# Optimization experiments

Measured on AMD Instinct MI355X. Metric: run time of the kernel, lower is better.

The kernel has to match this reference:

```python
import jax, jax.numpy as jnp
import numpy as np

N = 50000   # total nodes (50 graphs x 1000 nodes)
E = 500000  # total edges (avg degree 10)
G = 50      # number of graphs in the batch
IN = 128    # in_dim
H = 4       # attn_head
HID = [64, 128]  # graph_hiddens
SLOPE = 0.2      # negative_slope


def setup_inputs() -> dict:
    key = jax.random.key(0)
    ks = jax.random.split(key, 12)
    nodes_per_g = N // G
    edges_per_g = E // G
    # edges stay inside their own graph block (batched-graph structure)
    off = (jnp.arange(E) // edges_per_g) * nodes_per_g
    edge_src = (jax.random.randint(ks[0], (E,), 0, nodes_per_g) + off).astype(jnp.int32)
    edge_dst = (jax.random.randint(ks[1], (E,), 0, nodes_per_g) + off).astype(jnp.int32)
    node_graph = (jnp.arange(N) // nodes_per_g).astype(jnp.int32)

    def lin(k, i, o):
        return (jax.random.normal(k, (i, o), jnp.float32) / np.sqrt(i)).astype(jnp.float32)

    return dict(
        x=jax.random.normal(ks[2], (N, IN), jnp.float32),
        edge_src=edge_src, edge_dst=edge_dst, node_graph=node_graph,
        Wl1=lin(ks[3], IN, H * HID[0]), bl1=jnp.zeros((H * HID[0],), jnp.float32),
        Wr1=lin(ks[4], IN, H * HID[0]), br1=jnp.zeros((H * HID[0],), jnp.float32),
        attn1=jax.random.normal(ks[5], (H, HID[0]), jnp.float32) * 0.1,
        Wl2=lin(ks[6], HID[0], H * HID[1]), bl2=jnp.zeros((H * HID[1],), jnp.float32),
        Wr2=lin(ks[7], HID[0], H * HID[1]), br2=jnp.zeros((H * HID[1],), jnp.float32),
        attn2=jax.random.normal(ks[8], (H, HID[1]), jnp.float32) * 0.1,
        gate_w=lin(ks[9], HID[1], 1), gate_b=jnp.zeros((1,), jnp.float32),
    )


def _gat_layer(x, src, dst, Wl, bl, Wr, br, attn, n_heads, d_out):
    """DGL GATv2Conv (share_weights=False, no dropout) + maxpool over heads."""
    n = x.shape[0]
    fs = (x @ Wl + bl).reshape(n, n_heads, d_out)  # fc_src -> [N,H,D]
    fd = (x @ Wr + br).reshape(n, n_heads, d_out)  # fc_dst -> [N,H,D]
    # per-edge GATv2 logits: attn . leaky_relu(fs_u + fd_v)
    e = jax.nn.leaky_relu(fs[src] + fd[dst], SLOPE)      # [E,H,D]
    logits = jnp.einsum('ehd,hd->eh', e, attn)           # [E,H]
    # edge softmax over incoming edges of each destination node
    m = jax.ops.segment_max(logits, dst, num_segments=n)  # [N,H]
    a = jnp.exp(logits - m[dst])
    s = jax.ops.segment_sum(a, dst, num_segments=n)
    alpha = a / s[dst]                                   # [E,H]
    out = jax.ops.segment_sum(alpha[:, :, None] * fs[src], dst, num_segments=n)  # [N,H,D]
    # MaxPool1d(attn_head) over the head dimension -> [N,D]
    return out.max(axis=1)


def reference(x, edge_src, edge_dst, node_graph,
              Wl1, bl1, Wr1, br1, attn1,
              Wl2, bl2, Wr2, br2, attn2,
              gate_w, gate_b):
    h = _gat_layer(x, edge_src, edge_dst, Wl1, bl1, Wr1, br1, attn1, H, HID[0])
    h = _gat_layer(h, edge_src, edge_dst, Wl2, bl2, Wr2, br2, attn2, H, HID[1])
    # GlobalAttentionPooling: softmax(gate_nn(h)) per graph, weighted sum
    gate = (h @ gate_w + gate_b)[:, 0]                      # [N]
    gm = jax.ops.segment_max(gate, node_graph, num_segments=G)
    ga = jnp.exp(gate - gm[node_graph])
    gs = jax.ops.segment_sum(ga, node_graph, num_segments=G)
    alpha = (ga / gs[node_graph])[:, None]                  # [N,1]
    return jax.ops.segment_sum(alpha * h, node_graph, num_segments=G)  # [G, HID[1]]
```

## Files before the change

kernel.cpp:

```cpp
#include <hip/hip_runtime.h>
#include <hip/hip_bf16.h>


#define NN 50000
#define EE 500000
#define GG 50
#define NPG 1000
#define HH 4

typedef unsigned short ushort_t;
typedef unsigned int uint_t;
typedef __attribute__((ext_vector_type(8))) short bf16x8;
typedef __attribute__((ext_vector_type(4))) float f32x4;
typedef __attribute__((ext_vector_type(2))) float f32x2;

__device__ __forceinline__ ushort_t bf16r(float f) {
  __hip_bfloat16 h = __float2bfloat16(f);
  return *reinterpret_cast<ushort_t*>(&h);
}

__device__ __forceinline__ f32x2 up2v(uint_t u) {
  f32x2 r;
  r.x = __uint_as_float(u << 16);
  r.y = __uint_as_float(u & 0xffff0000u);
  return r;
}


__global__ void count_dst(const int* __restrict__ dst, int* __restrict__ counts) {
  int i = blockIdx.x * 256 + threadIdx.x;
  if (i < EE) atomicAdd(&counts[dst[i]], 1);
}

__global__ void scan_block(const int* __restrict__ in, int* __restrict__ out,
                           int* __restrict__ bsum, int n) {
  __shared__ int tmp[256];
  int t = threadIdx.x;
  int i = blockIdx.x * 256 + t;
  int v = (i < n) ? in[i] : 0;
  tmp[t] = v;
  __syncthreads();
  for (int off = 1; off < 256; off <<= 1) {
    int a = (t >= off) ? tmp[t - off] : 0;
    __syncthreads();
    tmp[t] += a;
    __syncthreads();
  }
  if (i < n) out[i] = tmp[t] - v;
  if (t == 255) bsum[blockIdx.x] = tmp[t];
}

__global__ void scan_bsum(int* __restrict__ bsum, int nb) {
  __shared__ int tmp[256];
  int t = threadIdx.x;
  int v = (t < nb) ? bsum[t] : 0;
  tmp[t] = v;
  __syncthreads();
  for (int off = 1; off < 256; off <<= 1) {
    int a = (t >= off) ? tmp[t - off] : 0;
    __syncthreads();
    tmp[t] += a;
    __syncthreads();
  }
  if (t < nb) bsum[t] = tmp[t] - v;
}

__global__ void scan_add(int* __restrict__ out, const int* __restrict__ bsum,
                         int* __restrict__ cursor, int n) {
  int i = blockIdx.x * 256 + threadIdx.x;
  if (i < n) {
    out[i] += bsum[blockIdx.x];
    cursor[i] = 0;
  }
}

__global__ void scatter_edges(const int* __restrict__ src, const int* __restrict__ dst,
                              const int* __restrict__ rowstart, int* __restrict__ cursor,
                              int* __restrict__ csr_src) {
  int i = blockIdx.x * 256 + threadIdx.x;
  if (i < EE) {
    int d = dst[i];
    int p = atomicAdd(&cursor[d], 1);
    csr_src[rowstart[d] + p] = src[i];
  }
}


__global__ void prep_w_all(const float* __restrict__ Wl1, const float* __restrict__ Wr1,
                           const float* __restrict__ Wl2, const float* __restrict__ Wr2,
                           ushort_t* __restrict__ BW1, ushort_t* __restrict__ BW2) {
  int i = blockIdx.x * 256 + threadIdx.x;
  if (i < 512 * 128) {
    int n = i >> 7, k = i & 127;
    const float* W = (n < 256) ? Wl1 : Wr1;
    BW1[i] = bf16r(W[(size_t)k * 256 + (n & 255)]);
  } else {
    int j = i - 512 * 128;
    int n = j >> 6, k = j & 63;
    const float* W = (n < 512) ? Wl2 : Wr2;
    BW2[j] = bf16r(W[(size_t)k * 512 + (n & 511)]);
  }
}


template<int KDIM, bool AF32>
__global__ __launch_bounds__(256)
void gemm_mfma(const float* __restrict__ Af, const ushort_t* __restrict__ Ab,
               const ushort_t* __restrict__ BW,
               const float* __restrict__ bl, const float* __restrict__ br, int nhalf,
               ushort_t* __restrict__ C, int nstride) {
  constexpr int RS = 72;
  __shared__ __align__(16) ushort_t As[128 * RS];
  __shared__ __align__(16) ushort_t Bs[128 * RS];
  const int t = threadIdx.x;
  const int m0 = blockIdx.x * 128, n0 = blockIdx.y * 128;
  const int lane = t & 63, wv = t >> 6;
  const int l16 = lane & 15, quad = lane >> 4;

  f32x4 acc[2][8];
#pragma unroll
  for (int b = 0; b < 2; ++b)
#pragma unroll
    for (int n = 0; n < 8; ++n) acc[b][n] = (f32x4){0.f, 0.f, 0.f, 0.f};

  for (int k0 = 0; k0 < KDIM; k0 += 64) {
    __syncthreads();
    if (AF32) {
      const int r = t >> 4, c4 = t & 15;
#pragma unroll
      for (int p = 0; p < 8; ++p) {
        int m = m0 + r + p * 16;
        int ms = (m < NN) ? m : NN - 1;
        float4 v = *(const float4*)(Af + (size_t)ms * KDIM + k0 + c4 * 4);
        uint2 pk;
        pk.x = (uint_t)bf16r(v.x) | ((uint_t)bf16r(v.y) << 16);
        pk.y = (uint_t)bf16r(v.z) | ((uint_t)bf16r(v.w) << 16);
        *(uint2*)(As + (r + p * 16) * RS + c4 * 4) = pk;
      }
    } else {
      const int r = t >> 3, seg = t & 7;
#pragma unroll
      for (int p = 0; p < 4; ++p) {
        int m = m0 + r + p * 32;
        int ms = (m < NN) ? m : NN - 1;
        *(uint4*)(As + (r + p * 32) * RS + seg * 8) =
            *(const uint4*)(Ab + (size_t)ms * KDIM + k0 + seg * 8);
      }
    }
    {
      const int r = t >> 3, seg = t & 7;
#pragma unroll
      for (int p = 0; p < 4; ++p) {
        *(uint4*)(Bs + (r + p * 32) * RS + seg * 8) =
            *(const uint4*)(BW + (size_t)(n0 + r + p * 32) * KDIM + k0 + seg * 8);
      }
    }
    __syncthreads();
#pragma unroll
    for (int kk = 0; kk < 2; ++kk) {
      bf16x8 a[2];
#pragma unroll
      for (int b = 0; b < 2; ++b)
        a[b] = *(const bf16x8*)(As + (wv * 32 + b * 16 + l16) * RS + kk * 32 + quad * 8);
#pragma unroll
      for (int n = 0; n < 8; ++n) {
        bf16x8 bb = *(const bf16x8*)(Bs + (n * 16 + l16) * RS + kk * 32 + quad * 8);
        acc[0][n] = __builtin_amdgcn_mfma_f32_16x16x32_bf16(a[0], bb, acc[0][n], 0, 0, 0);
        acc[1][n] = __builtin_amdgcn_mfma_f32_16x16x32_bf16(a[1], bb, acc[1][n], 0, 0, 0);
      }
    }
  }
  const float* bp = (n0 < nhalf) ? bl : br;
  const int nb = (n0 < nhalf) ? n0 : n0 - nhalf;
#pragma unroll
  for (int n = 0; n < 8; ++n) {
    const int col = n0 + n * 16 + l16;
    const float bv = bp[nb + n * 16 + l16];
#pragma unroll
    for (int b = 0; b < 2; ++b) {
      const int rowb = m0 + wv * 32 + b * 16 + quad * 4;
#pragma unroll
      for (int r = 0; r < 4; ++r) {
        if (rowb + r < NN)
          C[(size_t)(rowb + r) * nstride + col] = bf16r(acc[b][n][r] + bv);
      }
    }
  }
}


template<int N32> struct UV;
template<> struct UV<2> { typedef uint2 T; };
template<> struct UV<4> { typedef uint4 T; };

#define GAT_SLOTS ((NN / 4 + 7) / 8)
#define GAT_GRID  (GAT_SLOTS * 8)

template<int D, int STRIDE, bool OUTBF, bool GATE>
__global__ __launch_bounds__(256)
void gat_layer(const ushort_t* __restrict__ fsb, const ushort_t* __restrict__ fdb,
               const float* __restrict__ attn,
               const int* __restrict__ rowstart, const int* __restrict__ deg,
               const int* __restrict__ csr_src,
               float4* __restrict__ out4, ushort_t* __restrict__ outb,
               const float* __restrict__ gw, float* __restrict__ gate) {
  constexpr int DPL = D / 16;
  constexpr int NU  = DPL / 2;
  constexpr int NV4 = DPL / 4;
  constexpr int D4  = D / 4;
  typedef typename UV<NU>::T LT;

  const int b    = blockIdx.x;
  const int slot = (b & 7) * GAT_SLOTS + (b >> 3);
  if (slot >= NN / 4) return;
  const int lane = threadIdx.x & 63;
  const int wvid = threadIdx.x >> 6;
  const int v    = (slot << 2) + wvid;
  const int h    = lane >> 4;
  const int g16  = lane & 15;
  const int foff = h * D + g16 * DPL;

  f32x2 at2[NU], fd2[NU], gw2[NU];
  {
    const float* ap = attn + foff;
#pragma unroll
    for (int j = 0; j < NU; ++j) { at2[j].x = ap[2 * j]; at2[j].y = ap[2 * j + 1]; }
    LT raw = *reinterpret_cast<const LT*>(fdb + (size_t)v * STRIDE + foff);
    const uint_t* rw = reinterpret_cast<const uint_t*>(&raw);
#pragma unroll
    for (int j = 0; j < NU; ++j) fd2[j] = up2v(rw[j]);
    if constexpr (GATE) {
      const float* gp = gw + g16 * DPL;
#pragma unroll
      for (int j = 0; j < NU; ++j) { gw2[j].x = gp[2 * j]; gw2[j].y = gp[2 * j + 1]; }
    }
  }
  const int start = rowstart[v];
  const int n     = deg[v];
  const int* cp   = csr_src + start;

  float s = 0.f;
  f32x2 acc2[NU];
#pragma unroll
  for (int j = 0; j < NU; ++j) acc2[j] = (f32x2){0.f, 0.f};

  for (int e = 0; e < n; ++e) {
    const int u = cp[e];
    LT raw = *reinterpret_cast<const LT*>(fsb + (size_t)u * STRIDE + foff);
    const uint_t* rw = reinterpret_cast<const uint_t*>(&raw);
    f32x2 f0[NU];
#pragma unroll
    for (int j = 0; j < NU; ++j) f0[j] = up2v(rw[j]);
    f32x2 p2 = (f32x2){0.f, 0.f};
#pragma unroll
    for (int j = 0; j < NU; ++j) {
      f32x2 t = f0[j] + fd2[j];
      f32x2 l = __builtin_elementwise_max(t, t * 0.2f);
      p2 = __builtin_elementwise_fma(l, at2[j], p2);
    }
    float p = p2.x + p2.y;
    p += __shfl_xor(p, 1);
    p += __shfl_xor(p, 2);
    p += __shfl_xor(p, 4);
    p += __shfl_xor(p, 8);
    const float w = __expf(p);
    s += w;
    const f32x2 wv2 = {w, w};
#pragma unroll
    for (int j = 0; j < NU; ++j)
      acc2[j] = __builtin_elementwise_fma(wv2, f0[j], acc2[j]);
  }

  const float rs = (n > 0) ? (1.0f / s) : 0.f;
  float acc[DPL];
#pragma unroll
  for (int j = 0; j < NU; ++j) {
    acc[2 * j]     = acc2[j].x * rs;
    acc[2 * j + 1] = acc2[j].y * rs;
  }
#pragma unroll
  for (int i = 0; i < DPL; ++i) {
    acc[i] = fmaxf(acc[i], __shfl_xor(acc[i], 16));
    acc[i] = fmaxf(acc[i], __shfl_xor(acc[i], 32));
  }
  if constexpr (GATE) {
    f32x2 g2 = (f32x2){0.f, 0.f};
#pragma unroll
    for (int j = 0; j < NU; ++j) {
      f32x2 a2; a2.x = acc[2 * j]; a2.y = acc[2 * j + 1];
      g2 = __builtin_elementwise_fma(a2, gw2[j], g2);
    }
    float gp = g2.x + g2.y;
    gp += __shfl_xor(gp, 1);  gp += __shfl_xor(gp, 2);  gp += __shfl_xor(gp, 4);
    gp += __shfl_xor(gp, 8);  gp += __shfl_xor(gp, 16); gp += __shfl_xor(gp, 32);
    if (lane == 0) gate[v] = gp * 0.25f;
  }
  if (h == 0) {
    if constexpr (OUTBF) {
      ushort4 o;
      o.x = bf16r(acc[0]); o.y = bf16r(acc[1]); o.z = bf16r(acc[2]); o.w = bf16r(acc[3]);
      *reinterpret_cast<ushort4*>(outb + (size_t)v * D + g16 * 4) = o;
    } else {
#pragma unroll
      for (int i = 0; i < NV4; ++i)
        out4[(size_t)v * D4 + g16 * NV4 + i] =
            make_float4(acc[4 * i], acc[4 * i + 1], acc[4 * i + 2], acc[4 * i + 3]);
    }
  }
}


__global__ __launch_bounds__(256)
void pool_soft(const float* __restrict__ gate, float* __restrict__ alpha) {
  const int g = blockIdx.x, t = threadIdx.x;
  const int lane = t & 63, w = t >> 6;
  __shared__ float red[4];
  __shared__ float finm, fins;
  const float* gp = gate + g * NPG;

  float m = -__builtin_inff();
  for (int i = t; i < NPG; i += 256) m = fmaxf(m, gp[i]);
  m = fmaxf(m, __shfl_xor(m, 1));  m = fmaxf(m, __shfl_xor(m, 2));
  m = fmaxf(m, __shfl_xor(m, 4));  m = fmaxf(m, __shfl_xor(m, 8));
  m = fmaxf(m, __shfl_xor(m, 16)); m = fmaxf(m, __shfl_xor(m, 32));
  if (lane == 0) red[w] = m;
  __syncthreads();
  if (t == 0) finm = fmaxf(fmaxf(red[0], red[1]), fmaxf(red[2], red[3]));
  __syncthreads();
  const float gm = finm;

  float s = 0.f;
  for (int i = t; i < NPG; i += 256) s += __expf(gp[i] - gm);
  s += __shfl_xor(s, 1);  s += __shfl_xor(s, 2);  s += __shfl_xor(s, 4);
  s += __shfl_xor(s, 8);  s += __shfl_xor(s, 16); s += __shfl_xor(s, 32);
  if (lane == 0) red[w] = s;
  __syncthreads();
  if (t == 0) fins = 1.0f / (red[0] + red[1] + red[2] + red[3]);
  __syncthreads();
  const float inv = fins;

  for (int i = t; i < NPG; i += 256)
    alpha[g * NPG + i] = __expf(gp[i] - gm) * inv;
}

#define PCH 8
__global__ __launch_bounds__(128)
void pool_acc(const float* __restrict__ h2, const float* __restrict__ alpha,
              float* __restrict__ out) {
  const int g = blockIdx.x / PCH;
  const int c = blockIdx.x % PCH;
  const int d = threadIdx.x;
  const int n0 = g * NPG + c * (NPG / PCH);
  float acc = 0.f;
#pragma unroll 4
  for (int i = 0; i < NPG / PCH; ++i)
    acc = fmaf(alpha[n0 + i], h2[(size_t)(n0 + i) * 128 + d], acc);
  atomicAdd(&out[g * 128 + d], acc);
}


extern "C" void kernel_launch(void* const* d_in, const int* in_sizes, int n_in,
                              void* d_out, int out_size, void* d_ws, size_t ws_size,
                              hipStream_t stream) {
  const float* x        = (const float*)d_in[0];
  const int*   edge_src = (const int*)d_in[1];
  const int*   edge_dst = (const int*)d_in[2];
  const float* Wl1   = (const float*)d_in[4];
  const float* bl1   = (const float*)d_in[5];
  const float* Wr1   = (const float*)d_in[6];
  const float* br1   = (const float*)d_in[7];
  const float* attn1 = (const float*)d_in[8];
  const float* Wl2   = (const float*)d_in[9];
  const float* bl2   = (const float*)d_in[10];
  const float* Wr2   = (const float*)d_in[11];
  const float* br2   = (const float*)d_in[12];
  const float* attn2 = (const float*)d_in[13];
  const float* gate_w = (const float*)d_in[14];
  float* out = (float*)d_out;

  ushort_t* fsd1 = (ushort_t*)d_ws;
  ushort_t* fsd2 = fsd1;
  ushort_t* h1b  = fsd2 + (size_t)NN * 1024;
  float* h2      = (float*)(h1b + (size_t)NN * 64);
  float* gate    = h2 + (size_t)NN * 128;
  float* alpha   = gate + NN;
  ushort_t* BW1  = (ushort_t*)(alpha + NN);
  ushort_t* BW2  = BW1 + 512 * 128;
  int* counts   = (int*)(BW2 + 1024 * 64);
  int* rowstart = counts + NN;
  int* cursor   = rowstart + NN;
  int* csr_src  = cursor + NN;
  int* bsum     = csr_src + EE;

  hipMemsetAsync(counts, 0, NN * sizeof(int), stream);
  hipMemsetAsync(d_out, 0, (size_t)GG * 128 * sizeof(float), stream);

  const int nbN = (NN + 255) / 256;
  const int nbE = (EE + 255) / 256;
  const int MB  = (NN + 127) / 128;

  prep_w_all<<<(512 * 128 + 1024 * 64) / 256, 256, 0, stream>>>(
      Wl1, Wr1, Wl2, Wr2, BW1, BW2);

  count_dst<<<nbE, 256, 0, stream>>>(edge_dst, counts);
  scan_block<<<nbN, 256, 0, stream>>>(counts, rowstart, bsum, NN);
  scan_bsum<<<1, 256, 0, stream>>>(bsum, nbN);
  scan_add<<<nbN, 256, 0, stream>>>(rowstart, bsum, cursor, NN);
  scatter_edges<<<nbE, 256, 0, stream>>>(edge_src, edge_dst, rowstart, cursor, csr_src);

  gemm_mfma<128, true><<<dim3(MB, 4), 256, 0, stream>>>(
      x, nullptr, BW1, bl1, br1, 256, fsd1, 512);
  gat_layer<64, 512, true, false><<<GAT_GRID, 256, 0, stream>>>(
      fsd1, fsd1 + 256, attn1, rowstart, counts, csr_src,
      nullptr, h1b, nullptr, nullptr);
  gemm_mfma<64, false><<<dim3(MB, 8), 256, 0, stream>>>(
      nullptr, h1b, BW2, bl2, br2, 512, fsd2, 1024);
  gat_layer<128, 1024, false, true><<<GAT_GRID, 256, 0, stream>>>(
      fsd2, fsd2 + 512, attn2, rowstart, counts, csr_src,
      (float4*)h2, nullptr, gate_w, gate);

  pool_soft<<<GG, 256, 0, stream>>>(gate, alpha);
  pool_acc<<<GG * PCH, 128, 0, stream>>>(h2, alpha, out);
}
```

Before: 408.7 us.

## Fuse prep kernels and pooling kernels, prefetch neighbor rows in GAT loop

Merges the weight-conversion kernel into the degree-count kernel and merges the two pooling kernels into one 1024-thread kernel per graph. That kernel keeps alpha in shared memory and writes the output directly, so the alpha buffer, the output memset and the atomics are gone. The GAT edge loop now software-prefetches the next neighbor row and makes rowstart/deg wave-uniform with readfirstlane, and the gate weights are loaded late to reduce register pressure. The aim is fewer launches and better latency hiding. The cost is only 50 blocks for pooling and possibly more registers from the prefetch.

```diff
diff --git a/kernel.cpp b/kernel.cpp
--- a/kernel.cpp
+++ b/kernel.cpp
@@ -7,6 +7,8 @@
 #define GG 50
 #define NPG 1000
 #define HH 4
+#define NB_E ((EE + 255) / 256)
+#define NB_W 512
 
 typedef unsigned short ushort_t;
 typedef unsigned int uint_t;
@@ -27,10 +29,29 @@
 }
 
 
-__global__ void count_dst(const int* __restrict__ dst, int* __restrict__ counts) {
-  int i = blockIdx.x * 256 + threadIdx.x;
-  if (i < EE) atomicAdd(&counts[dst[i]], 1);
-}
+__global__ void prep_count(const int* __restrict__ dst, int* __restrict__ counts,
+                           const float* __restrict__ Wl1, const float* __restrict__ Wr1,
+                           const float* __restrict__ Wl2, const float* __restrict__ Wr2,
+                           ushort_t* __restrict__ BW1, ushort_t* __restrict__ BW2) {
+  const int b = blockIdx.x;
+  if (b < NB_E) {
+    int i = b * 256 + threadIdx.x;
+    if (i < EE) atomicAdd(&counts[dst[i]], 1);
+  } else {
+    int i = (b - NB_E) * 256 + threadIdx.x;
+    if (i < 512 * 128) {
+      int n = i >> 7, k = i & 127;
+      const float* W = (n < 256) ? Wl1 : Wr1;
+      BW1[i] = bf16r(W[(size_t)k * 256 + (n & 255)]);
+    } else {
+      int j = i - 512 * 128;
+      int n = j >> 6, k = j & 63;
+      const float* W = (n < 512) ? Wl2 : Wr2;
+      BW2[j] = bf16r(W[(size_t)k * 512 + (n & 511)]);
+    }
+  }
+}
+
 
 __global__ void scan_block(const int* __restrict__ in, int* __restrict__ out,
                            int* __restrict__ bsum, int n) {
@@ -82,23 +103,6 @@
     int d = dst[i];
     int p = atomicAdd(&cursor[d], 1);
     csr_src[rowstart[d] + p] = src[i];
-  }
-}
-
-
-__global__ void prep_w_all(const float* __restrict__ Wl1, const float* __restrict__ Wr1,
-                           const float* __restrict__ Wl2, const float* __restrict__ Wr2,
-                           ushort_t* __restrict__ BW1, ushort_t* __restrict__ BW2) {
-  int i = blockIdx.x * 256 + threadIdx.x;
-  if (i < 512 * 128) {
-    int n = i >> 7, k = i & 127;
-    const float* W = (n < 256) ? Wl1 : Wr1;
-    BW1[i] = bf16r(W[(size_t)k * 256 + (n & 255)]);
-  } else {
-    int j = i - 512 * 128;
-    int n = j >> 6, k = j & 63;
-    const float* W = (n < 512) ? Wl2 : Wr2;
-    BW2[j] = bf16r(W[(size_t)k * 512 + (n & 511)]);
   }
 }
 
@@ -220,7 +224,7 @@
   const int g16  = lane & 15;
   const int foff = h * D + g16 * DPL;
 
-  f32x2 at2[NU], fd2[NU], gw2[NU];
+  f32x2 at2[NU], fd2[NU];
   {
     const float* ap = attn + foff;
 #pragma unroll
@@ -229,14 +233,9 @@
     const uint_t* rw = reinterpret_cast<const uint_t*>(&raw);
 #pragma unroll
     for (int j = 0; j < NU; ++j) fd2[j] = up2v(rw[j]);
-    if constexpr (GATE) {
-      const float* gp = gw + g16 * DPL;
-#pragma unroll
-      for (int j = 0; j < NU; ++j) { gw2[j].x = gp[2 * j]; gw2[j].y = gp[2 * j + 1]; }
-    }
-  }
-  const int start = rowstart[v];
-  const int n     = deg[v];
+  }
+  const int start = __builtin_amdgcn_readfirstlane(rowstart[v]);
+  const int n     = __builtin_amdgcn_readfirstlane(deg[v]);
   const int* cp   = csr_src + start;
 
   float s = 0.f;
@@ -244,31 +243,35 @@
 #pragma unroll
   for (int j = 0; j < NU; ++j) acc2[j] = (f32x2){0.f, 0.f};
 
-  for (int e = 0; e < n; ++e) {
-    const int u = cp[e];
-    LT raw = *reinterpret_cast<const LT*>(fsb + (size_t)u * STRIDE + foff);
-    const uint_t* rw = reinterpret_cast<const uint_t*>(&raw);
-    f32x2 f0[NU];
-#pragma unroll
-    for (int j = 0; j < NU; ++j) f0[j] = up2v(rw[j]);
-    f32x2 p2 = (f32x2){0.f, 0.f};
-#pragma unroll
-    for (int j = 0; j < NU; ++j) {
-      f32x2 t = f0[j] + fd2[j];
-      f32x2 l = __builtin_elementwise_max(t, t * 0.2f);
-      p2 = __builtin_elementwise_fma(l, at2[j], p2);
-    }
-    float p = p2.x + p2.y;
-    p += __shfl_xor(p, 1);
-    p += __shfl_xor(p, 2);
-    p += __shfl_xor(p, 4);
-    p += __shfl_xor(p, 8);
-    const float w = __expf(p);
-    s += w;
-    const f32x2 wv2 = {w, w};
-#pragma unroll
-    for (int j = 0; j < NU; ++j)
-      acc2[j] = __builtin_elementwise_fma(wv2, f0[j], acc2[j]);
+  if (n > 0) {
+    LT raw = *reinterpret_cast<const LT*>(fsb + (size_t)cp[0] * STRIDE + foff);
+    for (int e = 1; e <= n; ++e) {
+      const LT cur = raw;
+      if (e < n)
+        raw = *reinterpret_cast<const LT*>(fsb + (size_t)cp[e] * STRIDE + foff);
+      const uint_t* rw = reinterpret_cast<const uint_t*>(&cur);
+      f32x2 f0[NU];
+#pragma unroll
+      for (int j = 0; j < NU; ++j) f0[j] = up2v(rw[j]);
+      f32x2 p2 = (f32x2){0.f, 0.f};
+#pragma unroll
+      for (int j = 0; j < NU; ++j) {
+        f32x2 t = f0[j] + fd2[j];
+        f32x2 l = __builtin_elementwise_max(t, t * 0.2f);
+        p2 = __builtin_elementwise_fma(l, at2[j], p2);
+      }
+      float p = p2.x + p2.y;
+      p += __shfl_xor(p, 1);
+      p += __shfl_xor(p, 2);
+      p += __shfl_xor(p, 4);
+      p += __shfl_xor(p, 8);
+      const float w = __expf(p);
+      s += w;
+      const f32x2 wv2 = {w, w};
+#pragma unroll
+      for (int j = 0; j < NU; ++j)
+        acc2[j] = __builtin_elementwise_fma(wv2, f0[j], acc2[j]);
+    }
   }
 
   const float rs = (n > 0) ? (1.0f / s) : 0.f;
@@ -284,16 +287,13 @@
     acc[i] = fmaxf(acc[i], __shfl_xor(acc[i], 32));
   }
   if constexpr (GATE) {
-    f32x2 g2 = (f32x2){0.f, 0.f};
-#pragma unroll
-    for (int j = 0; j < NU; ++j) {
-      f32x2 a2; a2.x = acc[2 * j]; a2.y = acc[2 * j + 1];
-      g2 = __builtin_elementwise_fma(a2, gw2[j], g2);
-    }
-    float gp = g2.x + g2.y;
-    gp += __shfl_xor(gp, 1);  gp += __shfl_xor(gp, 2);  gp += __shfl_xor(gp, 4);
-    gp += __shfl_xor(gp, 8);  gp += __shfl_xor(gp, 16); gp += __shfl_xor(gp, 32);
-    if (lane == 0) gate[v] = gp * 0.25f;
+    const float* gp = gw + g16 * DPL;
+    float g = 0.f;
+#pragma unroll
+    for (int i = 0; i < DPL; ++i) g = fmaf(acc[i], gp[i], g);
+    g += __shfl_xor(g, 1);  g += __shfl_xor(g, 2);  g += __shfl_xor(g, 4);
+    g += __shfl_xor(g, 8);  g += __shfl_xor(g, 16); g += __shfl_xor(g, 32);
+    if (lane == 0) gate[v] = g * 0.25f;
   }
   if (h == 0) {
     if constexpr (OUTBF) {
@@ -310,52 +310,61 @@
 }
 
 
-__global__ __launch_bounds__(256)
-void pool_soft(const float* __restrict__ gate, float* __restrict__ alpha) {
+__global__ __launch_bounds__(1024)
+void pool_fused(const float* __restrict__ gate, const float* __restrict__ h2,
+                float* __restrict__ out) {
   const int g = blockIdx.x, t = threadIdx.x;
   const int lane = t & 63, w = t >> 6;
-  __shared__ float red[4];
-  __shared__ float finm, fins;
-  const float* gp = gate + g * NPG;
-
-  float m = -__builtin_inff();
-  for (int i = t; i < NPG; i += 256) m = fmaxf(m, gp[i]);
+  __shared__ float a_s[NPG];
+  __shared__ float red[16];
+  __shared__ float fin;
+  __shared__ float part[8][128];
+
+  float gv = (t < NPG) ? gate[g * NPG + t] : -__builtin_inff();
+  float m = gv;
   m = fmaxf(m, __shfl_xor(m, 1));  m = fmaxf(m, __shfl_xor(m, 2));
   m = fmaxf(m, __shfl_xor(m, 4));  m = fmaxf(m, __shfl_xor(m, 8));
   m = fmaxf(m, __shfl_xor(m, 16)); m = fmaxf(m, __shfl_xor(m, 32));
   if (lane == 0) red[w] = m;
   __syncthreads();
-  if (t == 0) finm = fmaxf(fmaxf(red[0], red[1]), fmaxf(red[2], red[3]));
-  __syncthreads();
-  const float gm = finm;
-
-  float s = 0.f;
-  for (int i = t; i < NPG; i += 256) s += __expf(gp[i] - gm);
+  if (t == 0) {
+    float r = red[0];
+#pragma unroll
+    for (int j = 1; j < 16; ++j) r = fmaxf(r, red[j]);
+    fin = r;
+  }
+  __syncthreads();
+  const float gm = fin;
+
+  float ex = (t < NPG) ? __expf(gv - gm) : 0.f;
+  float s = ex;
   s += __shfl_xor(s, 1);  s += __shfl_xor(s, 2);  s += __shfl_xor(s, 4);
   s += __shfl_xor(s, 8);  s += __shfl_xor(s, 16); s += __shfl_xor(s, 32);
   if (lane == 0) red[w] = s;
   __syncthreads();
-  if (t == 0) fins = 1.0f / (red[0] + red[1] + red[2] + red[3]);
-  __syncthreads();
-  const float inv = fins;
-
-  for (int i = t; i < NPG; i += 256)
-    alpha[g * NPG + i] = __expf(gp[i] - gm) * inv;
-}
-
-#define PCH 8
-__global__ __launch_bounds__(128)
-void pool_acc(const float* __restrict__ h2, const float* __restrict__ alpha,
-              float* __restrict__ out) {
-  const int g = blockIdx.x / PCH;
-  const int c = blockIdx.x % PCH;
-  const int d = threadIdx.x;
-  const int n0 = g * NPG + c * (NPG / PCH);
+  if (t == 0) {
+    float r = 0.f;
+#pragma unroll
+    for (int j = 0; j < 16; ++j) r += red[j];
+    fin = 1.0f / r;
+  }
+  __syncthreads();
+  if (t < NPG) a_s[t] = ex * fin;
+  __syncthreads();
+
+  const int d = t & 127;
+  const int c = t >> 7;
   float acc = 0.f;
-#pragma unroll 4
-  for (int i = 0; i < NPG / PCH; ++i)
-    acc = fmaf(alpha[n0 + i], h2[(size_t)(n0 + i) * 128 + d], acc);
-  atomicAdd(&out[g * 128 + d], acc);
+  for (int i = c; i < NPG; i += 8)
+    acc = fmaf(a_s[i], h2[(size_t)(g * NPG + i) * 128 + d], acc);
+  part[c][d] = acc;
+  __syncthreads();
+  if (c == 0) {
+    float r = acc;
+#pragma unroll
+    for (int j = 1; j < 8; ++j) r += part[j][d];
+    out[g * 128 + d] = r;
+  }
 }
 
 
@@ -383,8 +392,7 @@
   ushort_t* h1b  = fsd2 + (size_t)NN * 1024;
   float* h2      = (float*)(h1b + (size_t)NN * 64);
   float* gate    = h2 + (size_t)NN * 128;
-  float* alpha   = gate + NN;
-  ushort_t* BW1  = (ushort_t*)(alpha + NN);
+  ushort_t* BW1  = (ushort_t*)(gate + NN);
   ushort_t* BW2  = BW1 + 512 * 128;
   int* counts   = (int*)(BW2 + 1024 * 64);
   int* rowstart = counts + NN;
@@ -393,16 +401,13 @@
   int* bsum     = csr_src + EE;
 
   hipMemsetAsync(counts, 0, NN * sizeof(int), stream);
-  hipMemsetAsync(d_out, 0, (size_t)GG * 128 * sizeof(float), stream);
 
   const int nbN = (NN + 255) / 256;
-  const int nbE = (EE + 255) / 256;
+  const int nbE = NB_E;
   const int MB  = (NN + 127) / 128;
 
-  prep_w_all<<<(512 * 128 + 1024 * 64) / 256, 256, 0, stream>>>(
-      Wl1, Wr1, Wl2, Wr2, BW1, BW2);
-
-  count_dst<<<nbE, 256, 0, stream>>>(edge_dst, counts);
+  prep_count<<<NB_E + NB_W, 256, 0, stream>>>(
+      edge_dst, counts, Wl1, Wr1, Wl2, Wr2, BW1, BW2);
   scan_block<<<nbN, 256, 0, stream>>>(counts, rowstart, bsum, NN);
   scan_bsum<<<1, 256, 0, stream>>>(bsum, nbN);
   scan_add<<<nbN, 256, 0, stream>>>(rowstart, bsum, cursor, NN);
@@ -419,6 +424,5 @@
       fsd2, fsd2 + 512, attn2, rowstart, counts, csr_src,
       (float4*)h2, nullptr, gate_w, gate);
 
-  pool_soft<<<GG, 256, 0, stream>>>(gate, alpha);
-  pool_acc<<<GG * PCH, 128, 0, stream>>>(h2, alpha, out);
-}
+  pool_fused<<<GG, 1024, 0, stream>>>(gate, h2, out);
+}
```

After: 377.1 us. -7.7%, faster.
